# Kernel tuning notes

Hardware: AMD Instinct MI355X
Metric: run time of the kernel (lower is better)

## Reference

```python
import jax, jax.numpy as jnp
import numpy as np

COMMITMENT = 0.25
EPS = 1e-10


def setup_inputs() -> dict:
    key = jax.random.key(0)
    k1, k2 = jax.random.split(key)
    x = jax.random.normal(k1, (16, 16384, 64), dtype=jnp.float32)
    embed = jax.random.normal(k2, (64, 512), dtype=jnp.float32)  # [embed_dim, n_embed]
    sigma = jnp.ones((1,), dtype=jnp.float32)
    return {"x": x, "embed": embed, "sigma": sigma}


def reference(x, embed, sigma):
    # x: [B, T, D]; embed: [D, K]; sigma: [1]
    D, K = embed.shape
    flat = x.reshape(-1, D)  # [N, D]
    dist = (jnp.sum(flat * flat, axis=1, keepdims=True)
            - 2.0 * (flat @ embed)
            + jnp.sum(embed * embed, axis=0, keepdims=True))
    soft_assign = jax.nn.softmax(-sigma * dist, axis=1)  # [N, K]
    likelihoods = jnp.mean(soft_assign, axis=0)          # [K]
    embed_ind = jnp.argmax(soft_assign, axis=1)          # [N]
    hard = jnp.take(embed.T, embed_ind, axis=0)          # [N, D] gather of codewords
    soft_proj = soft_assign @ embed.T                    # [N, D]
    # straight-through: forward = hard, backward = soft path
    quantize = (soft_proj + jax.lax.stop_gradient(hard - soft_proj)).reshape(x.shape)
    # KL(uniform || likelihoods.detach()), batchmean over K, scaled by commitment
    p = 1.0 / K
    ql = jax.lax.stop_gradient(likelihoods)
    quant_loss = COMMITMENT * jnp.mean(p * (jnp.log(p) - jnp.log(ql + EPS)))
    return quantize, quant_loss, likelihoods
```

## Files before the change

### kernel.cpp

```cpp
#include <hip/hip_runtime.h>

#define NROWS    262144
#define DIMS     64
#define KCODES   512
#define MTILE    32
#define RPW      4
#define CHUNK    256
#define NCHUNK   2
#define D_PER    16
#define D_CHUNKS 4
#define NTHREADS 512

__global__ void prep_kernel(const float* __restrict__ embed,
                            float* __restrict__ embedT,
                            float* __restrict__ enorm,
                            float* __restrict__ lik) {
    int k = blockIdx.x;
    int d = threadIdx.x;
    float v = embed[d * KCODES + k];
    embedT[k * DIMS + d] = v;
    float sq = __fmul_rn(v, v);
    int j = d & 7;
    float r = __shfl(sq, j, 64);
#pragma unroll
    for (int i = 1; i < 8; ++i)
        r = __fadd_rn(r, __shfl(sq, j + 8 * i, 64));
    float t;
    t = __shfl_xor(r, 1, 64); r = __fadd_rn(r, t);
    t = __shfl_xor(r, 2, 64); r = __fadd_rn(r, t);
    t = __shfl_xor(r, 4, 64); r = __fadd_rn(r, t);
    if (d == 0) { enorm[k] = r; lik[k] = 0.0f; }
}

__launch_bounds__(NTHREADS)
__global__ void main_kernel(const float* __restrict__ x,
                            const float* __restrict__ embed,
                            const float* __restrict__ sigma,
                            const float* __restrict__ embedT,
                            const float* __restrict__ enorm,
                            float* __restrict__ lik,
                            float* __restrict__ out) {
    __shared__ float e_lds[D_PER * KCODES];

    const int tid = threadIdx.x;
    const int cg  = tid & 63;
    const int rg  = tid >> 6;
    const int rowbase = blockIdx.x * MTILE + rg * RPW;

    const float sigma_v = sigma[0];

    float acc[NCHUNK][RPW][4];
#pragma unroll
    for (int c = 0; c < NCHUNK; ++c)
#pragma unroll
        for (int r = 0; r < RPW; ++r)
#pragma unroll
            for (int q = 0; q < 4; ++q) acc[c][r][q] = 0.0f;

    const float2* __restrict__ x2  = reinterpret_cast<const float2*>(x);
    const float4* __restrict__ eg4 = reinterpret_cast<const float4*>(embed);
    float4* e_lds4 = reinterpret_cast<float4*>(e_lds);

    for (int dc = 0; dc < D_CHUNKS; ++dc) {
        __syncthreads();
#pragma unroll
        for (int i = 0; i < 4; ++i) {
            int f4 = tid + i * NTHREADS;
            e_lds4[f4] = eg4[dc * (D_PER * KCODES / 4) + f4];
        }
        __syncthreads();

        const float4* e4 = reinterpret_cast<const float4*>(e_lds);
#pragma unroll 2
        for (int d2 = 0; d2 < D_PER / 2; ++d2) {
            float4 e0a = e4[(2 * d2 + 0) * 128 +  0 + cg];
            float4 e1a = e4[(2 * d2 + 1) * 128 +  0 + cg];
            float4 e0b = e4[(2 * d2 + 0) * 128 + 64 + cg];
            float4 e1b = e4[(2 * d2 + 1) * 128 + 64 + cg];
            int d2g = dc * (D_PER / 2) + d2;
#pragma unroll
            for (int r = 0; r < RPW; ++r) {
                float2 xv = x2[(size_t)(rowbase + r) * 32 + d2g];
                acc[0][r][0] = fmaf(xv.x, e0a.x, acc[0][r][0]);
                acc[0][r][1] = fmaf(xv.x, e0a.y, acc[0][r][1]);
                acc[0][r][2] = fmaf(xv.x, e0a.z, acc[0][r][2]);
                acc[0][r][3] = fmaf(xv.x, e0a.w, acc[0][r][3]);
                acc[0][r][0] = fmaf(xv.y, e1a.x, acc[0][r][0]);
                acc[0][r][1] = fmaf(xv.y, e1a.y, acc[0][r][1]);
                acc[0][r][2] = fmaf(xv.y, e1a.z, acc[0][r][2]);
                acc[0][r][3] = fmaf(xv.y, e1a.w, acc[0][r][3]);
                acc[1][r][0] = fmaf(xv.x, e0b.x, acc[1][r][0]);
                acc[1][r][1] = fmaf(xv.x, e0b.y, acc[1][r][1]);
                acc[1][r][2] = fmaf(xv.x, e0b.z, acc[1][r][2]);
                acc[1][r][3] = fmaf(xv.x, e0b.w, acc[1][r][3]);
                acc[1][r][0] = fmaf(xv.y, e1b.x, acc[1][r][0]);
                acc[1][r][1] = fmaf(xv.y, e1b.y, acc[1][r][1]);
                acc[1][r][2] = fmaf(xv.y, e1b.z, acc[1][r][2]);
                acc[1][r][3] = fmaf(xv.y, e1b.w, acc[1][r][3]);
            }
        }
    }

    const int r_l = (cg >> 3) & 3;
    const int j_l = cg & 7;
    float xr;
    {
        const float* xp = x + (size_t)(rowbase + r_l) * DIMS + j_l;
        float v0 = xp[0];
        float s = __fmul_rn(v0, v0);
#pragma unroll
        for (int i = 1; i < 8; ++i) {
            float v = xp[8 * i];
            s = __fadd_rn(s, __fmul_rn(v, v));
        }
        xr = s;
    }
    {
        float t;
        t = __shfl_xor(xr, 1, 64); xr = __fadd_rn(xr, t);
        t = __shfl_xor(xr, 2, 64); xr = __fadd_rn(xr, t);
        t = __shfl_xor(xr, 4, 64); xr = __fadd_rn(xr, t);
    }

    float en[NCHUNK][4];
#pragma unroll
    for (int c = 0; c < NCHUNK; ++c)
#pragma unroll
        for (int q = 0; q < 4; ++q)
            en[c][q] = enorm[c * CHUNK + cg * 4 + q];

    float likpart[NCHUNK][4];
#pragma unroll
    for (int c = 0; c < NCHUNK; ++c)
#pragma unroll
        for (int q = 0; q < 4; ++q) likpart[c][q] = 0.0f;

#pragma unroll
    for (int r = 0; r < RPW; ++r) {
        float xn = __shfl(xr, r * 8, 64);
        float m = -INFINITY;
#pragma unroll
        for (int c = 0; c < NCHUNK; ++c)
#pragma unroll
            for (int q = 0; q < 4; ++q) {
                float dot  = acc[c][r][q];
                float td   = __fsub_rn(xn, __fmul_rn(2.0f, dot));
                float dist = __fadd_rn(td, en[c][q]);
                float zz   = __fmul_rn(-sigma_v, dist);
                acc[c][r][q] = zz;
                m = fmaxf(m, zz);
            }
#pragma unroll
        for (int mask = 1; mask < 64; mask <<= 1)
            m = fmaxf(m, __shfl_xor(m, mask, 64));

        float s = 0.0f;
        float bv = -1.0f;
        int   bc = KCODES;
#pragma unroll
        for (int c = 0; c < NCHUNK; ++c)
#pragma unroll
            for (int q = 0; q < 4; ++q) {
                float ee = expf(__fsub_rn(acc[c][r][q], m));
                acc[c][r][q] = ee;
                s += ee;
                int col = c * CHUNK + cg * 4 + q;
                if (ee > bv) { bv = ee; bc = col; }
            }
#pragma unroll
        for (int mask = 1; mask < 64; mask <<= 1)
            s += __shfl_xor(s, mask, 64);
#pragma unroll
        for (int mask = 1; mask < 64; mask <<= 1) {
            float ov = __shfl_xor(bv, mask, 64);
            int   oc = __shfl_xor(bc, mask, 64);
            if (ov > bv || (ov == bv && oc < bc)) { bv = ov; bc = oc; }
        }

        float invS = 1.0f / s;
#pragma unroll
        for (int c = 0; c < NCHUNK; ++c)
#pragma unroll
            for (int q = 0; q < 4; ++q)
                likpart[c][q] = fmaf(acc[c][r][q], invS, likpart[c][q]);

        int row = rowbase + r;
        __builtin_nontemporal_store(embedT[bc * DIMS + cg],
                                    &out[(size_t)row * DIMS + cg]);
    }

    float* red = e_lds;
    __syncthreads();
    red[tid] = 0.0f;
    __syncthreads();
#pragma unroll
    for (int c = 0; c < NCHUNK; ++c)
#pragma unroll
        for (int q = 0; q < 4; ++q)
            atomicAdd(&red[c * CHUNK + cg * 4 + q], likpart[c][q]);
    __syncthreads();
    atomicAdd(&lik[tid], red[tid]);
}

__global__ void finish_kernel(const float* __restrict__ lik,
                              float* __restrict__ out) {
    int tid = threadIdx.x;
    float l = lik[tid] / 262144.0f;
    out[16777217 + tid] = l;
    const float p = 1.0f / 512.0f;
    float term = __fmul_rn(p, __fsub_rn(logf(p), logf(l + 1e-10f)));
#pragma unroll
    for (int mask = 1; mask < 64; mask <<= 1)
        term += __shfl_xor(term, mask, 64);
    __shared__ float ws[8];
    if ((tid & 63) == 0) ws[tid >> 6] = term;
    __syncthreads();
    if (tid == 0) {
        float ssum = 0.0f;
        for (int i = 0; i < 8; ++i) ssum += ws[i];
        out[16777216] = 0.25f * (ssum / 512.0f);
    }
}

extern "C" void kernel_launch(void* const* d_in, const int* in_sizes, int n_in,
                              void* d_out, int out_size, void* d_ws, size_t ws_size,
                              hipStream_t stream) {
    const float* x     = (const float*)d_in[0];
    const float* embed = (const float*)d_in[1];
    const float* sigma = (const float*)d_in[2];
    float* out = (float*)d_out;
    float* ws  = (float*)d_ws;

    float* embedT = ws;
    float* enorm  = ws + 32768;
    float* lik    = ws + 33280;

    prep_kernel<<<KCODES, DIMS, 0, stream>>>(embed, embedT, enorm, lik);
    main_kernel<<<NROWS / MTILE, NTHREADS, 0, stream>>>(x, embed, sigma,
                                                        embedT, enorm, lik, out);
    finish_kernel<<<1, NTHREADS, 0, stream>>>(lik, out);
}
```

Before: 553.8 us.

## Use packed FMA, DPP lane swaps, and ballot-based argmax in VQ kernel

Switches the distance accumulators to two-wide float vectors so the compiler can emit packed FP32 FMA instructions, halving the FMA instruction count in the inner dot-product loop. Replaces the first two butterfly steps of the wave reductions with DPP quad-permute moves instead of ds_bpermute shuffles. Replaces the shuffle-based argmax reduction with a ballot over lanes whose exponential equals one (the max element), picking the lowest column. This removes a long chain of paired shuffles, but the tie-breaking relies on exp(0) being exactly 1 and on lane order matching column order within each chunk.

```diff
diff --git a/kernel.cpp b/kernel.cpp
--- a/kernel.cpp
+++ b/kernel.cpp
@@ -10,6 +10,17 @@
 #define D_PER    16
 #define D_CHUNKS 4
 #define NTHREADS 512
+
+typedef float v2f __attribute__((ext_vector_type(2)));
+
+__device__ __forceinline__ float dpp_xor1(float v) {
+    int i = __builtin_amdgcn_update_dpp(0, __float_as_int(v), 0xB1, 0xF, 0xF, true);
+    return __int_as_float(i);
+}
+__device__ __forceinline__ float dpp_xor2(float v) {
+    int i = __builtin_amdgcn_update_dpp(0, __float_as_int(v), 0x4E, 0xF, 0xF, true);
+    return __int_as_float(i);
+}
 
 __global__ void prep_kernel(const float* __restrict__ embed,
                             float* __restrict__ embedT,
@@ -49,13 +60,13 @@
 
     const float sigma_v = sigma[0];
 
-    float acc[NCHUNK][RPW][4];
+    v2f acc[NCHUNK][RPW][2];
 #pragma unroll
     for (int c = 0; c < NCHUNK; ++c)
 #pragma unroll
         for (int r = 0; r < RPW; ++r)
 #pragma unroll
-            for (int q = 0; q < 4; ++q) acc[c][r][q] = 0.0f;
+            for (int p = 0; p < 2; ++p) acc[c][r][p] = (v2f){0.0f, 0.0f};
 
     const float2* __restrict__ x2  = reinterpret_cast<const float2*>(x);
     const float4* __restrict__ eg4 = reinterpret_cast<const float4*>(embed);
@@ -71,32 +82,31 @@
         __syncthreads();
 
         const float4* e4 = reinterpret_cast<const float4*>(e_lds);
+        const int dbase = dc * (D_PER / 2);
 #pragma unroll 2
         for (int d2 = 0; d2 < D_PER / 2; ++d2) {
             float4 e0a = e4[(2 * d2 + 0) * 128 +  0 + cg];
             float4 e1a = e4[(2 * d2 + 1) * 128 +  0 + cg];
             float4 e0b = e4[(2 * d2 + 0) * 128 + 64 + cg];
             float4 e1b = e4[(2 * d2 + 1) * 128 + 64 + cg];
-            int d2g = dc * (D_PER / 2) + d2;
+            v2f e0al = {e0a.x, e0a.y}, e0ah = {e0a.z, e0a.w};
+            v2f e1al = {e1a.x, e1a.y}, e1ah = {e1a.z, e1a.w};
+            v2f e0bl = {e0b.x, e0b.y}, e0bh = {e0b.z, e0b.w};
+            v2f e1bl = {e1b.x, e1b.y}, e1bh = {e1b.z, e1b.w};
+            int d2g = dbase + d2;
 #pragma unroll
             for (int r = 0; r < RPW; ++r) {
                 float2 xv = x2[(size_t)(rowbase + r) * 32 + d2g];
-                acc[0][r][0] = fmaf(xv.x, e0a.x, acc[0][r][0]);
-                acc[0][r][1] = fmaf(xv.x, e0a.y, acc[0][r][1]);
-                acc[0][r][2] = fmaf(xv.x, e0a.z, acc[0][r][2]);
-                acc[0][r][3] = fmaf(xv.x, e0a.w, acc[0][r][3]);
-                acc[0][r][0] = fmaf(xv.y, e1a.x, acc[0][r][0]);
-                acc[0][r][1] = fmaf(xv.y, e1a.y, acc[0][r][1]);
-                acc[0][r][2] = fmaf(xv.y, e1a.z, acc[0][r][2]);
-                acc[0][r][3] = fmaf(xv.y, e1a.w, acc[0][r][3]);
-                acc[1][r][0] = fmaf(xv.x, e0b.x, acc[1][r][0]);
-                acc[1][r][1] = fmaf(xv.x, e0b.y, acc[1][r][1]);
-                acc[1][r][2] = fmaf(xv.x, e0b.z, acc[1][r][2]);
-                acc[1][r][3] = fmaf(xv.x, e0b.w, acc[1][r][3]);
-                acc[1][r][0] = fmaf(xv.y, e1b.x, acc[1][r][0]);
-                acc[1][r][1] = fmaf(xv.y, e1b.y, acc[1][r][1]);
-                acc[1][r][2] = fmaf(xv.y, e1b.z, acc[1][r][2]);
-                acc[1][r][3] = fmaf(xv.y, e1b.w, acc[1][r][3]);
+                v2f xx = {xv.x, xv.x};
+                v2f xy = {xv.y, xv.y};
+                acc[0][r][0] = __builtin_elementwise_fma(xx, e0al, acc[0][r][0]);
+                acc[0][r][1] = __builtin_elementwise_fma(xx, e0ah, acc[0][r][1]);
+                acc[0][r][0] = __builtin_elementwise_fma(xy, e1al, acc[0][r][0]);
+                acc[0][r][1] = __builtin_elementwise_fma(xy, e1ah, acc[0][r][1]);
+                acc[1][r][0] = __builtin_elementwise_fma(xx, e0bl, acc[1][r][0]);
+                acc[1][r][1] = __builtin_elementwise_fma(xx, e0bh, acc[1][r][1]);
+                acc[1][r][0] = __builtin_elementwise_fma(xy, e1bl, acc[1][r][0]);
+                acc[1][r][1] = __builtin_elementwise_fma(xy, e1bh, acc[1][r][1]);
             }
         }
     }
@@ -117,8 +127,8 @@
     }
     {
         float t;
-        t = __shfl_xor(xr, 1, 64); xr = __fadd_rn(xr, t);
-        t = __shfl_xor(xr, 2, 64); xr = __fadd_rn(xr, t);
+        t = dpp_xor1(xr);          xr = __fadd_rn(xr, t);
+        t = dpp_xor2(xr);          xr = __fadd_rn(xr, t);
         t = __shfl_xor(xr, 4, 64); xr = __fadd_rn(xr, t);
     }
 
@@ -134,6 +144,8 @@
     for (int c = 0; c < NCHUNK; ++c)
 #pragma unroll
         for (int q = 0; q < 4; ++q) likpart[c][q] = 0.0f;
+
+#define ACC(c, r, q) (acc[c][r][(q) >> 1][(q) & 1])
 
 #pragma unroll
     for (int r = 0; r < RPW; ++r) {
@@ -143,51 +155,56 @@
         for (int c = 0; c < NCHUNK; ++c)
 #pragma unroll
             for (int q = 0; q < 4; ++q) {
-                float dot  = acc[c][r][q];
+                float dot  = ACC(c, r, q);
                 float td   = __fsub_rn(xn, __fmul_rn(2.0f, dot));
                 float dist = __fadd_rn(td, en[c][q]);
                 float zz   = __fmul_rn(-sigma_v, dist);
-                acc[c][r][q] = zz;
+                ACC(c, r, q) = zz;
                 m = fmaxf(m, zz);
             }
-#pragma unroll
-        for (int mask = 1; mask < 64; mask <<= 1)
-            m = fmaxf(m, __shfl_xor(m, mask, 64));
+        m = fmaxf(m, dpp_xor1(m));
+        m = fmaxf(m, dpp_xor2(m));
+        m = fmaxf(m, __shfl_xor(m,  4, 64));
+        m = fmaxf(m, __shfl_xor(m,  8, 64));
+        m = fmaxf(m, __shfl_xor(m, 16, 64));
+        m = fmaxf(m, __shfl_xor(m, 32, 64));
 
         float s = 0.0f;
-        float bv = -1.0f;
-        int   bc = KCODES;
+        int lcol = 1024;
 #pragma unroll
         for (int c = 0; c < NCHUNK; ++c)
 #pragma unroll
             for (int q = 0; q < 4; ++q) {
-                float ee = expf(__fsub_rn(acc[c][r][q], m));
-                acc[c][r][q] = ee;
+                float ee = expf(__fsub_rn(ACC(c, r, q), m));
+                ACC(c, r, q) = ee;
                 s += ee;
                 int col = c * CHUNK + cg * 4 + q;
-                if (ee > bv) { bv = ee; bc = col; }
+                lcol = (ee == 1.0f) ? min(lcol, col) : lcol;
             }
-#pragma unroll
-        for (int mask = 1; mask < 64; mask <<= 1)
-            s += __shfl_xor(s, mask, 64);
-#pragma unroll
-        for (int mask = 1; mask < 64; mask <<= 1) {
-            float ov = __shfl_xor(bv, mask, 64);
-            int   oc = __shfl_xor(bc, mask, 64);
-            if (ov > bv || (ov == bv && oc < bc)) { bv = ov; bc = oc; }
-        }
+        unsigned long long b0 = __ballot(lcol < CHUNK);
+        unsigned long long ba = __ballot(lcol < 1024);
+        int srcl = (int)(b0 ? __ffsll(b0) : __ffsll(ba)) - 1;
+        int bc = __shfl(lcol, srcl, 64);
+
+        s = __fadd_rn(s, dpp_xor1(s));
+        s = __fadd_rn(s, dpp_xor2(s));
+        s = __fadd_rn(s, __shfl_xor(s,  4, 64));
+        s = __fadd_rn(s, __shfl_xor(s,  8, 64));
+        s = __fadd_rn(s, __shfl_xor(s, 16, 64));
+        s = __fadd_rn(s, __shfl_xor(s, 32, 64));
 
         float invS = 1.0f / s;
 #pragma unroll
         for (int c = 0; c < NCHUNK; ++c)
 #pragma unroll
             for (int q = 0; q < 4; ++q)
-                likpart[c][q] = fmaf(acc[c][r][q], invS, likpart[c][q]);
+                likpart[c][q] = fmaf(ACC(c, r, q), invS, likpart[c][q]);
 
         int row = rowbase + r;
         __builtin_nontemporal_store(embedT[bc * DIMS + cg],
                                     &out[(size_t)row * DIMS + cg]);
     }
+#undef ACC
 
     float* red = e_lds;
     __syncthreads();
```

Result: no change. 562.4 us (+1.5%).
